# Performance work log

Hardware: AMD Instinct MI355X
Metric: run time of the kernel (lower is better)

## Reference

```python
import numpy as np
import jax
import jax.numpy as jnp
from collections import deque

NUM_CLASSES = 32
N_PARENTS = 4
N_CHILD = 7
SINK_WEIGHT = 0.1
EPS = 1e-7
B, D, H, W = 2, 96, 96, 96

# ---- static tree construction (mirrors adjacency_matrix / bitpack_tree / reachability) ----

def _build_adjacency():
    n = NUM_CLASSES + 1  # node 0 is the virtual root
    A = np.zeros((n, n), dtype=np.int64)
    for p in range(N_PARENTS):
        A[0, 1 + p] = 1
        for c in range(N_CHILD):
            A[1 + p, 1 + N_PARENTS + p * N_CHILD + c] = 1
    return A

ADJ = _build_adjacency()

def _reachability(A):
    # R[i, j] = 1 iff j is reachable from i (i is ancestor-or-self of j)
    R = np.eye(A.shape[0], dtype=bool) | (A > 0)
    for _ in range(A.shape[0]):
        Rn = R | (R @ (A > 0))
        if (Rn == R).all():
            break
        R = Rn
    return R

def _bitpack(A):
    # each node's bitmask encodes its path from the root; (x & group) == class tests descendant-ness
    n = A.shape[0]
    bc = np.zeros(n, dtype=np.int64)
    bg = np.zeros(n, dtype=np.int64)
    bit = 0
    q = deque([0])
    while q:
        p = q.popleft()
        ch = np.nonzero(A[p])[0]
        if len(ch) == 0:
            continue
        w = int(np.ceil(np.log2(len(ch) + 1)))
        for i, c in enumerate(ch):
            bc[c] = bc[p] | ((i + 1) << bit)
            bg[c] = bg[p] | (((1 << w) - 1) << bit)
            q.append(c)
        bit += w
    return bc, bg

_BC, _BG = _bitpack(ADJ)
BM_CLASS = _BC[1:].astype(np.int32)
BM_GROUP = _BG[1:].astype(np.int32)
RMT = _reachability(ADJ)[1:, 1:].T.astype(np.float32)  # RMT[label, c] = c is ancestor-or-self
LEAF = np.nonzero(ADJ[1:, 1:].sum(axis=1) == 0)[0].astype(np.int32)
_SIB = ((ADJ.T @ ADJ) > 0)[1:, 1:]
SINK_IDS = [N_PARENTS + p * N_CHILD for p in range(N_PARENTS)]
PARENT_OF = {s: int(ADJ[1:, 1:][:, s].argmax()) for s in SINK_IDS}
SIBS = {}
for _s in SINK_IDS:
    _row = _SIB[_s].copy()
    _row[_s] = False
    SIBS[_s] = np.nonzero(_row)[0].tolist()
# DDESC[l, c] = 1 iff class l is a descendant-or-self of class c (bitmask test)
DDESC = ((BM_CLASS[:, None] & BM_GROUP[None, :]) == BM_CLASS[None, :]).astype(np.float32)


def setup_inputs() -> dict:
    key = jax.random.key(0)
    k1, k2 = jax.random.split(key)
    images = jax.random.normal(k1, (B, NUM_CLASSES, D, H, W), dtype=jnp.float32)
    targets = jax.random.randint(k2, (B, D, H, W), 0, NUM_CLASSES, dtype=jnp.int32)
    masks = jnp.ones((B, NUM_CLASSES), dtype=bool)
    return {"images": images, "targets": targets, "masks": masks}


def reference(images, targets, masks):
    C = NUM_CLASSES
    probs = jax.nn.softmax(images, axis=1)  # activation_fn over class dim
    leaf = jnp.asarray(LEAF)
    pred = leaf[jnp.argmax(probs[:, LEAF], axis=1)]  # _argmax_leaves -> [B,D,H,W] int32
    bm_class = jnp.asarray(BM_CLASS)
    rmt = jnp.asarray(RMT)
    ddesc = jnp.asarray(DDESC)

    def per_sample(p, pr, y, m):
        p = p.reshape(C, -1).T          # [N, C] probabilities
        y = y.reshape(-1)
        pr = pr.reshape(-1)
        valid = y != 255
        vw = valid.astype(p.dtype)
        y_safe = jnp.where(valid, y, 0).astype(jnp.int32)
        mf = m.astype(p.dtype)

        # ---- sink dice (hierarchical sink/sibling logic) ----
        pred_bm = bm_class[pr]
        sds, fls = [], []
        for s in SINK_IDS:
            sib_mask = jnp.zeros_like(valid)
            for sib in SIBS[s]:
                sib_mask = sib_mask | (y_safe == sib) | ((~m[sib]) & (pr == sib))
            par = PARENT_OF[s]
            pmask = (pred_bm & int(BM_GROUP[par])) == int(BM_CLASS[par])
            tgt = (pmask & (~sib_mask)).astype(p.dtype) * vw
            pp = p[:, s] * vw
            inter = jnp.sum(pp * tgt)
            d = 1.0 - (2.0 * inter + 1e-5) / (jnp.sum(pp) + jnp.sum(tgt) + 1e-5)
            sds.append(d)
            fls.append((jnp.sum(sib_mask & valid) > 0).astype(p.dtype))
        sd = jnp.stack(sds)
        fl = jnp.stack(fls)
        cnt = fl.sum()
        sink_dice = SINK_WEIGHT * jnp.where(cnt > 0, jnp.sum(sd * fl) / jnp.maximum(cnt, 1.0), 0.0)

        # ---- main dice (smooth_nr=0) + hierarchical CE over masked classes ----
        t = rmt[y_safe]                 # [N, C] multi-hot (label + ancestors)
        wcol = vw[:, None]
        inter = jnp.sum(p * t * wcol, axis=0)
        denom = jnp.sum(p * wcol, axis=0) + jnp.sum(t * wcol, axis=0)
        dice_c = 1.0 - (2.0 * inter) / (denom + 1e-5)
        dice = jnp.sum(dice_c * mf) / jnp.maximum(mf.sum(), 1.0)

        logp = jnp.log(jnp.clip(p, EPS, 1.0 - EPS))
        ce = jnp.sum(-jnp.sum(t * logp * mf[None, :], axis=1) * vw) / jnp.maximum(vw.sum(), 1.0)

        # ---- confusion matrix via joint (pred, true) histogram + descendant matrix ----
        flat = pr.astype(jnp.int32) * C + y_safe
        hist = jnp.zeros((C * C,), p.dtype).at[flat].add(vw).reshape(C, C)  # [pred, true]
        tp = jnp.einsum('lc,lt,tc->c', ddesc, hist, ddesc)
        fp = jnp.einsum('lc,lt->c', ddesc, hist) - tp
        fn = jnp.einsum('lt,tc->c', hist, ddesc) - tp
        cm = jnp.stack([tp, fp, fn], axis=-1) * mf[:, None]
        return jnp.stack([ce, dice, sink_dice]), cm

    loss, cm = jax.vmap(per_sample)(probs, pred, targets, masks)
    return loss, cm, pred
```

## Files before the change

kernel.cpp:

```cpp
#include <hip/hip_runtime.h>

#define NC 32
#define NVOX (96*96*96)
#define NB 384
#define TPB 256

#define WS_CE     0
#define WS_SP     32
#define WS_SPT    64
#define WS_SINKI  96
#define WS_SIB    100
#define WS_TGT    104
#define WS_HIST   128
#define SLOT_STRIDE 1152
#define NSLOT     (2 * NB)
#define FINAL_OFF (NSLOT * SLOT_STRIDE)

__device__ __forceinline__ float wave_reduce(float v) {
    #pragma unroll
    for (int off = 32; off > 0; off >>= 1)
        v += __shfl_down(v, off, 64);
    return v;
}

__global__ __launch_bounds__(TPB) void voxel_kernel(
    const float* __restrict__ images,
    const int*   __restrict__ targets,
    const int*   __restrict__ masks,
    float* __restrict__ ws,
    float* __restrict__ pred_out)
{
    const int slot = blockIdx.x;
    const int b    = slot & 1;
    const int blk  = slot >> 1;
    const int tid  = threadIdx.x;

    __shared__ float s_hist[NC * NC];
    __shared__ float s_spt[NC];
    __shared__ float s_mf[NC];
    __shared__ float s_red[45];

    for (int i = tid; i < NC * NC; i += TPB) s_hist[i] = 0.f;
    if (tid < 45) s_red[tid] = 0.f;
    if (tid < NC) {
        s_spt[tid] = 0.f;
        s_mf[tid]  = (masks[b * NC + tid] != 0) ? 1.f : 0.f;
    }
    __syncthreads();

    const float* img  = images + (size_t)b * NC * NVOX;
    const int*   tgt  = targets + (size_t)b * NVOX;
    float*       pout = pred_out + (size_t)b * NVOX;
    float*       wsb  = ws + (size_t)slot * SLOT_STRIDE;

    float sp[NC];
    #pragma unroll
    for (int c = 0; c < NC; ++c) sp[c] = 0.f;
    float ce = 0.f;
    float sinkI[4] = {0.f, 0.f, 0.f, 0.f};
    float sibc[4]  = {0.f, 0.f, 0.f, 0.f};
    float tgtc[4]  = {0.f, 0.f, 0.f, 0.f};

    for (int v = blk * TPB + tid; v < NVOX; v += NB * TPB) {
        const int  y     = tgt[v];
        const bool valid = (y != 255);
        const int  ysafe = valid ? y : 0;
        const float vwf  = valid ? 1.f : 0.f;

        float e[NC];
        float sum  = 0.f;
        float best = -3.4e38f;
        int   pred = 4;
        #pragma unroll
        for (int c = 0; c < NC; ++c) {
            float x  = img[(size_t)c * NVOX + v];
            float ev = __expf(x);
            e[c] = ev;
            sum += ev;
            if (c >= 4 && x > best) { best = x; pred = c; }
        }
        const float rinv = 1.f / sum;
        pout[v] = (float)pred;

        const int pp = (pred - 4) / 7;
        const int py = (ysafe >= 4) ? (ysafe - 4) / 7 : -1;

        float pyv = 0.f, ppv = 0.f;
        #pragma unroll
        for (int c = 0; c < NC; ++c) {
            float pc = e[c] * rinv;
            sp[c] += pc * vwf;
            if (c == ysafe) pyv = pc;
            if (c == py)    ppv = pc;
        }

        float term = __logf(fminf(fmaxf(pyv, 1e-7f), 1.f - 1e-7f)) * s_mf[ysafe];
        if (py >= 0)
            term += __logf(fminf(fmaxf(ppv, 1e-7f), 1.f - 1e-7f)) * s_mf[py];
        ce -= term * vwf;

        atomicAdd(&s_spt[ysafe], pyv * vwf);
        if (py >= 0) atomicAdd(&s_spt[py], ppv * vwf);

        atomicAdd(&s_hist[pred * NC + ysafe], vwf);

        const bool predMasked = (s_mf[pred] == 0.f);
        #pragma unroll
        for (int k = 0; k < 4; ++k) {
            const int  sk   = 4 + 7 * k;
            const bool ysib = (py == k) && (ysafe != sk);
            const bool msib = predMasked && (pp == k) && (pred != sk);
            const bool sib  = ysib || msib;
            if (sib && valid) sibc[k] += 1.f;
            const bool tg = (pp == k) && !sib && valid;
            if (tg) {
                tgtc[k]  += 1.f;
                sinkI[k] += e[sk] * rinv;
            }
        }
    }

    const int lane = tid & 63;
    {
        float r = wave_reduce(ce);
        if (lane == 0) atomicAdd(&s_red[0], r);
    }
    #pragma unroll
    for (int c = 0; c < NC; ++c) {
        float r = wave_reduce(sp[c]);
        if (lane == 0) atomicAdd(&s_red[1 + c], r);
    }
    #pragma unroll
    for (int k = 0; k < 4; ++k) {
        float r = wave_reduce(sinkI[k]);
        if (lane == 0) atomicAdd(&s_red[33 + k], r);
        r = wave_reduce(sibc[k]);
        if (lane == 0) atomicAdd(&s_red[37 + k], r);
        r = wave_reduce(tgtc[k]);
        if (lane == 0) atomicAdd(&s_red[41 + k], r);
    }
    __syncthreads();

    for (int i = tid; i < NC * NC; i += TPB) wsb[WS_HIST + i] = s_hist[i];
    if (tid == 0) wsb[WS_CE] = s_red[0];
    if (tid < NC) {
        wsb[WS_SP  + tid] = s_red[1 + tid];
        wsb[WS_SPT + tid] = s_spt[tid];
    }
    if (tid < 4) {
        wsb[WS_SINKI + tid] = s_red[33 + tid];
        wsb[WS_SIB   + tid] = s_red[37 + tid];
        wsb[WS_TGT   + tid] = s_red[41 + tid];
    }
}

__global__ __launch_bounds__(TPB) void reduce_kernel(
    const float* __restrict__ ws, float* __restrict__ wsf)
{
    const int g = blockIdx.x * TPB + threadIdx.x;
    if (g >= 2 * SLOT_STRIDE) return;
    const int b   = g / SLOT_STRIDE;
    const int val = g % SLOT_STRIDE;
    float s = 0.f;
    for (int blk = 0; blk < NB; ++blk)
        s += ws[(size_t)(2 * blk + b) * SLOT_STRIDE + val];
    wsf[(size_t)b * SLOT_STRIDE + val] = s;
}

__global__ __launch_bounds__(64) void finalize_kernel(
    const float* __restrict__ wsf,
    const int*   __restrict__ masks,
    float* __restrict__ out)
{
    const int b = blockIdx.x;
    const float* wsb  = wsf + (size_t)b * SLOT_STRIDE;
    const float* hist = wsb + WS_HIST;
    const int tid = threadIdx.x;

    __shared__ float s_col[NC], s_row[NC], s_dice[NC], s_mf[NC];

    if (tid < NC) {
        float cs = 0.f, rs = 0.f;
        for (int j = 0; j < NC; ++j) {
            cs += hist[j * NC + tid];
            rs += hist[tid * NC + j];
        }
        s_col[tid] = cs;
        s_row[tid] = rs;
        s_mf[tid]  = (masks[b * NC + tid] != 0) ? 1.f : 0.f;
    }
    __syncthreads();

    if (tid < NC) {
        const int c = tid;
        float ycnt, pcnt, tp;
        if (c < 4) {
            int idx[8];
            idx[0] = c;
            for (int j = 0; j < 7; ++j) idx[1 + j] = 4 + 7 * c + j;
            ycnt = s_col[c]; pcnt = s_row[c];
            for (int j = 0; j < 7; ++j) { ycnt += s_col[idx[1 + j]]; pcnt += s_row[idx[1 + j]]; }
            tp = 0.f;
            for (int a = 0; a < 8; ++a)
                for (int d = 0; d < 8; ++d)
                    tp += hist[idx[a] * NC + idx[d]];
        } else {
            ycnt = s_col[c]; pcnt = s_row[c];
            tp = hist[c * NC + c];
        }
        const float mf = s_mf[c];
        out[6 + (b * NC + c) * 3 + 0] = tp * mf;
        out[6 + (b * NC + c) * 3 + 1] = (pcnt - tp) * mf;
        out[6 + (b * NC + c) * 3 + 2] = (ycnt - tp) * mf;
        float dc = 1.f - 2.f * wsb[WS_SPT + c] / (wsb[WS_SP + c] + ycnt + 1e-5f);
        s_dice[c] = dc * mf;
    }
    __syncthreads();

    if (tid == 0) {
        float vw = 0.f, dsum = 0.f, msum = 0.f;
        for (int c = 0; c < NC; ++c) {
            vw   += s_col[c];
            dsum += s_dice[c];
            msum += s_mf[c];
        }
        const float ce   = wsb[WS_CE] / fmaxf(vw, 1.f);
        const float dice = dsum / fmaxf(msum, 1.f);
        float cnt = 0.f, sd = 0.f;
        for (int k = 0; k < 4; ++k) {
            float fl = (wsb[WS_SIB + k] > 0.f) ? 1.f : 0.f;
            float d  = 1.f - (2.f * wsb[WS_SINKI + k] + 1e-5f) /
                             (wsb[WS_SP + 4 + 7 * k] + wsb[WS_TGT + k] + 1e-5f);
            cnt += fl;
            sd  += d * fl;
        }
        const float sink = (cnt > 0.f) ? 0.1f * (sd / fmaxf(cnt, 1.f)) : 0.f;
        out[b * 3 + 0] = ce;
        out[b * 3 + 1] = dice;
        out[b * 3 + 2] = sink;
    }
}

extern "C" void kernel_launch(void* const* d_in, const int* in_sizes, int n_in,
                              void* d_out, int out_size, void* d_ws, size_t ws_size,
                              hipStream_t stream) {
    const float* images  = (const float*)d_in[0];
    const int*   targets = (const int*)d_in[1];
    const int*   masks   = (const int*)d_in[2];
    float* out = (float*)d_out;
    float* ws  = (float*)d_ws;
    float* wsf = ws + FINAL_OFF;

    voxel_kernel<<<dim3(NSLOT), dim3(TPB), 0, stream>>>(
        images, targets, masks, ws, out + 6 + 2 * NC * 3);
    reduce_kernel<<<dim3((2 * SLOT_STRIDE + TPB - 1) / TPB), dim3(TPB), 0, stream>>>(ws, wsf);
    finalize_kernel<<<dim3(2), dim3(64), 0, stream>>>(wsf, masks, out);
}
```

Before: 367.8 us.

## Stage exp values in LDS, raise block count, and split partial reduction

The per-voxel exponentials move from a 32-entry register array into a per-thread LDS row, so the class probabilities can be read by index instead of through unrolled compare-and-select loops. This lowers register pressure, and launch bounds now ask for 4 blocks per CU. The block count rises from 384 to 512. The reduce kernel is split into 8 chunks along a second grid dimension that combine with atomics into a buffer zeroed by a memset. The cost is about 33 KB of LDS per block, which may itself cap occupancy, plus extra LDS traffic and one more launch for the memset.

```diff
diff --git a/kernel.cpp b/kernel.cpp
--- a/kernel.cpp
+++ b/kernel.cpp
@@ -2,8 +2,9 @@
 
 #define NC 32
 #define NVOX (96*96*96)
-#define NB 384
+#define NB 512
 #define TPB 256
+#define ROWS 33
 
 #define WS_CE     0
 #define WS_SP     32
@@ -15,6 +16,8 @@
 #define SLOT_STRIDE 1152
 #define NSLOT     (2 * NB)
 #define FINAL_OFF (NSLOT * SLOT_STRIDE)
+#define NCHUNK    8
+#define BLK_PER_CH (NB / NCHUNK)
 
 __device__ __forceinline__ float wave_reduce(float v) {
     #pragma unroll
@@ -23,7 +26,7 @@
     return v;
 }
 
-__global__ __launch_bounds__(TPB) void voxel_kernel(
+__global__ __launch_bounds__(TPB, 4) void voxel_kernel(
     const float* __restrict__ images,
     const int*   __restrict__ targets,
     const int*   __restrict__ masks,
@@ -35,6 +38,7 @@
     const int blk  = slot >> 1;
     const int tid  = threadIdx.x;
 
+    __shared__ float s_e[TPB * ROWS];
     __shared__ float s_hist[NC * NC];
     __shared__ float s_spt[NC];
     __shared__ float s_mf[NC];
@@ -52,6 +56,7 @@
     const int*   tgt  = targets + (size_t)b * NVOX;
     float*       pout = pred_out + (size_t)b * NVOX;
     float*       wsb  = ws + (size_t)slot * SLOT_STRIDE;
+    float*       et   = &s_e[tid * ROWS];
 
     float sp[NC];
     #pragma unroll
@@ -67,57 +72,58 @@
         const int  ysafe = valid ? y : 0;
         const float vwf  = valid ? 1.f : 0.f;
 
-        float e[NC];
         float sum  = 0.f;
         float best = -3.4e38f;
         int   pred = 4;
         #pragma unroll
         for (int c = 0; c < NC; ++c) {
-            float x  = img[(size_t)c * NVOX + v];
-            float ev = __expf(x);
-            e[c] = ev;
-            sum += ev;
-            if (c >= 4 && x > best) { best = x; pred = c; }
+            const float x  = img[(size_t)c * NVOX + v];
+            const float ev = __expf(x);
+            et[c] = ev;
+            sum  += ev;
+            if (c >= 4) {
+                if (x > best) { best = x; pred = c; }
+            }
         }
         const float rinv = 1.f / sum;
         pout[v] = (float)pred;
 
         const int pp = (pred - 4) / 7;
         const int py = (ysafe >= 4) ? (ysafe - 4) / 7 : -1;
-
-        float pyv = 0.f, ppv = 0.f;
-        #pragma unroll
-        for (int c = 0; c < NC; ++c) {
-            float pc = e[c] * rinv;
-            sp[c] += pc * vwf;
-            if (c == ysafe) pyv = pc;
-            if (c == py)    ppv = pc;
-        }
+        const int pyi = (py >= 0) ? py : 0;
+
+        const float pyv  = et[ysafe] * rinv;
+        const float ppv  = et[pyi] * rinv;
+        const float eskv = et[4 + 7 * pp] * rinv;
 
         float term = __logf(fminf(fmaxf(pyv, 1e-7f), 1.f - 1e-7f)) * s_mf[ysafe];
         if (py >= 0)
-            term += __logf(fminf(fmaxf(ppv, 1e-7f), 1.f - 1e-7f)) * s_mf[py];
+            term += __logf(fminf(fmaxf(ppv, 1e-7f), 1.f - 1e-7f)) * s_mf[pyi];
         ce -= term * vwf;
 
         atomicAdd(&s_spt[ysafe], pyv * vwf);
-        if (py >= 0) atomicAdd(&s_spt[py], ppv * vwf);
+        if (py >= 0) atomicAdd(&s_spt[pyi], ppv * vwf);
 
         atomicAdd(&s_hist[pred * NC + ysafe], vwf);
 
-        const bool predMasked = (s_mf[pred] == 0.f);
+        const bool pm = (s_mf[pred] == 0.f);
         #pragma unroll
         for (int k = 0; k < 4; ++k) {
             const int  sk   = 4 + 7 * k;
             const bool ysib = (py == k) && (ysafe != sk);
-            const bool msib = predMasked && (pp == k) && (pred != sk);
+            const bool msib = pm && (pp == k) && (pred != sk);
             const bool sib  = ysib || msib;
             if (sib && valid) sibc[k] += 1.f;
-            const bool tg = (pp == k) && !sib && valid;
-            if (tg) {
+            if ((pp == k) && !sib && valid) {
                 tgtc[k]  += 1.f;
-                sinkI[k] += e[sk] * rinv;
+                sinkI[k] += eskv;
             }
         }
+
+        const float rw = rinv * vwf;
+        #pragma unroll
+        for (int c = 0; c < NC; ++c)
+            sp[c] = __builtin_fmaf(et[c], rw, sp[c]);
     }
 
     const int lane = tid & 63;
@@ -157,14 +163,17 @@
 __global__ __launch_bounds__(TPB) void reduce_kernel(
     const float* __restrict__ ws, float* __restrict__ wsf)
 {
-    const int g = blockIdx.x * TPB + threadIdx.x;
-    if (g >= 2 * SLOT_STRIDE) return;
-    const int b   = g / SLOT_STRIDE;
-    const int val = g % SLOT_STRIDE;
+    const int v = blockIdx.x * TPB + threadIdx.x;
+    if (v >= 2 * SLOT_STRIDE) return;
+    const int b   = v / SLOT_STRIDE;
+    const int val = v % SLOT_STRIDE;
+    const int blk0 = blockIdx.y * BLK_PER_CH;
+    const float* base = ws + (size_t)b * SLOT_STRIDE + val;
     float s = 0.f;
-    for (int blk = 0; blk < NB; ++blk)
-        s += ws[(size_t)(2 * blk + b) * SLOT_STRIDE + val];
-    wsf[(size_t)b * SLOT_STRIDE + val] = s;
+    #pragma unroll 8
+    for (int i = 0; i < BLK_PER_CH; ++i)
+        s += base[(size_t)(2 * (blk0 + i)) * SLOT_STRIDE];
+    atomicAdd(&wsf[v], s);
 }
 
 __global__ __launch_bounds__(64) void finalize_kernel(
@@ -251,8 +260,10 @@
     float* ws  = (float*)d_ws;
     float* wsf = ws + FINAL_OFF;
 
+    hipMemsetAsync(wsf, 0, 2 * SLOT_STRIDE * sizeof(float), stream);
+
     voxel_kernel<<<dim3(NSLOT), dim3(TPB), 0, stream>>>(
         images, targets, masks, ws, out + 6 + 2 * NC * 3);
-    reduce_kernel<<<dim3((2 * SLOT_STRIDE + TPB - 1) / TPB), dim3(TPB), 0, stream>>>(ws, wsf);
+    reduce_kernel<<<dim3((2 * SLOT_STRIDE + TPB - 1) / TPB, NCHUNK), dim3(TPB), 0, stream>>>(ws, wsf);
     finalize_kernel<<<dim3(2), dim3(64), 0, stream>>>(wsf, masks, out);
 }
```

Measured after the change: 342.6 us. 1.07x faster.
